# Kernel tuning notes

Hardware: AMD Instinct MI355X
Metric: run time of the kernel (lower is better)

## Reference

```python
import jax, jax.numpy as jnp
import numpy as np

B, S, DIM = 1, 4096, 4096
H, HL, D = 32, 8, 128          # query heads, kv heads (GQA), head_dim
BS = 8                          # sparse_block_size
SINK_TOK, WIN_TOK = 30, 30
HEAVY = 800                     # heavy_const -> Mb = HEAVY // BS top blocks
NEG = -1e30


def setup_inputs() -> dict:
    key = jax.random.key(0)
    k0, k1, k2, k3 = jax.random.split(key, 4)
    x = jax.random.normal(k0, (B, S, DIM), jnp.float32)
    freqs_cis = jax.random.uniform(k1, (S, D // 2, 2), jnp.float32)  # (cos,sin)-like pairs
    wqkv_w = jax.random.normal(k2, ((H + 2 * HL) * D, DIM), jnp.float32) * 0.02
    wo_w = jax.random.normal(k3, (DIM, DIM), jnp.float32) * 0.02
    input_pos = jnp.arange(S, dtype=jnp.int32)
    return {"x": x, "freqs_cis": freqs_cis, "wqkv_w": wqkv_w, "wo_w": wo_w, "input_pos": input_pos}


def _rope(x, fc):
    # x: [B,S,h,D], fc: [S,D/2,2]
    xr = x.reshape(*x.shape[:-1], -1, 2)            # [B,S,h,D/2,2]
    fc = fc[None, :, None]                           # [1,S,1,D/2,2]
    out = jnp.stack([xr[..., 0] * fc[..., 0] - xr[..., 1] * fc[..., 1],
                     xr[..., 1] * fc[..., 0] + xr[..., 0] * fc[..., 1]], axis=-1)
    return out.reshape(x.shape)


def reference(x, freqs_cis, wqkv_w, wo_w, input_pos):
    rep = H // HL
    Tb = (S + BS - 1) // BS
    scale = 1.0 / jnp.sqrt(jnp.float32(D))

    qkv = x @ wqkv_w.T                               # [B,S,(H+2HL)*D]
    q, k, v = jnp.split(qkv, [H * D, (H + HL) * D], axis=-1)
    q = q.reshape(B, S, H, D)
    k = k.reshape(B, S, HL, D)
    v = v.reshape(B, S, HL, D)
    q = _rope(q, freqs_cis)
    k = _rope(k, freqs_cis)

    # ---- block accumulators (KVCache.update_tokens), vectorized ----
    blk = input_pos // BS                            # [S]
    k_sum = jax.ops.segment_sum(jnp.swapaxes(k, 0, 1), blk, num_segments=Tb)  # [Tb,B,HL,D]
    cnt = jax.ops.segment_sum(jnp.ones((S,), jnp.float32), blk, num_segments=Tb)  # [Tb]
    k_rep = k_sum / jnp.maximum(cnt, 1.0)[:, None, None, None]                # block-mean keys
    k_rep_h = jnp.repeat(k_rep, rep, axis=2)        # [Tb,B,H,D] (GQA repeat)

    # ---- per-(B,H) block routing scores ----
    q_mean = q.mean(axis=1)                          # [B,H,D]
    scores = jnp.einsum('bhd,tbhd->bht', q_mean, k_rep_h) * scale  # [B,H,Tb]
    scores = jnp.where(cnt[None, None, :] > 0, scores, NEG)

    # ---- build_block_index: sink + window + topk ----
    sink_b = min((min(SINK_TOK, S) + BS - 1) // BS, Tb)
    window_b = min((min(WIN_TOK, S) + BS - 1) // BS, Tb)
    cur_block = (S - 1) // BS
    win_start = max(0, cur_block - window_b + 1)
    win_end = cur_block + 1
    sink_ids = jnp.arange(sink_b, dtype=jnp.int32)
    window_ids = jnp.arange(win_start, win_end, dtype=jnp.int32)
    Mb = max(0, min(HEAVY // BS, Tb))
    sc = scores.at[..., :sink_b].set(NEG).at[..., window_ids].set(NEG)
    top_ids = jax.lax.top_k(sc, Mb)[1].astype(jnp.int32)                      # [B,H,Mb]
    bidx = jnp.concatenate([
        jnp.broadcast_to(sink_ids, (B, H, sink_b)),
        jnp.broadcast_to(window_ids, (B, H, win_end - win_start)),
        top_ids], axis=-1)                           # [B,H,KLIST]

    # ---- gather selected block tokens ----
    tok = bidx[..., None] * BS + jnp.arange(BS, dtype=jnp.int32)              # [B,H,KLIST,BS]
    KL = bidx.shape[-1]
    tok = tok.reshape(B, H, KL * BS)                 # [B,H,Kt]
    valid = (tok >= 0) & (tok < S)
    tok_c = jnp.clip(tok, 0, S - 1)

    k_bhsd = jnp.swapaxes(jnp.repeat(k, rep, axis=2), 1, 2)  # [B,H,S,D]
    v_bhsd = jnp.swapaxes(jnp.repeat(v, rep, axis=2), 1, 2)
    Ksel = jnp.take_along_axis(k_bhsd, tok_c[..., None], axis=2)  # [B,H,Kt,D]
    Vsel = jnp.take_along_axis(v_bhsd, tok_c[..., None], axis=2)

    # ---- block-sparse attention with causal mask ----
    q_bhsd = jnp.swapaxes(q, 1, 2)                   # [B,H,S,D]
    att = jnp.einsum('bhsd,bhkd->bhsk', q_bhsd, Ksel) * scale
    mask = (tok_c[:, :, None, :] <= input_pos[None, None, :, None]) & valid[:, :, None, :]
    att = jnp.where(mask, att, NEG)
    p = jax.nn.softmax(att, axis=-1)
    out = jnp.einsum('bhsk,bhkd->bhsd', p, Vsel)     # [B,H,S,D]
    y = jnp.swapaxes(out, 1, 2).reshape(B, S, H * D) @ wo_w.T
    return y
```

## Files before the change

### kernel.cpp

```cpp
#include <hip/hip_runtime.h>
#include <hip/hip_bf16.h>

typedef unsigned short u16;
typedef unsigned int   u32;

using bf16x8 = __attribute__((ext_vector_type(8))) short;
using f32x4  = __attribute__((ext_vector_type(4))) float;

constexpr int S = 4096, DIM = 4096, H = 32, HL = 8, D = 128;
constexpr int NQKV = (H + 2 * HL) * D;
constexpr int QVW = (H + HL) * D;
constexpr int TB = S / 8;
constexpr int KL = 108;
constexpr float NEGF = -1e30f;
constexpr float SCALE = 0.08838834764831845f;

__device__ inline float bflo(u32 u) { return __builtin_bit_cast(float, u << 16); }
__device__ inline float bfhi(u32 u) { return __builtin_bit_cast(float, u & 0xFFFF0000u); }
__device__ inline u16 rne16(float f) {
  u32 b = __builtin_bit_cast(u32, f);
  return (u16)((b + 0x7FFFu + ((b >> 16) & 1u)) >> 16);
}
__device__ inline float bf2f(u16 h) { return __builtin_bit_cast(float, (u32)h << 16); }
__device__ inline u32 pk2(u16 a, u16 b) { return (u32)a | ((u32)b << 16); }

__device__ __forceinline__ void gload16(const u16* g, u16* l) {
  __builtin_amdgcn_global_load_lds(
      (__attribute__((address_space(1))) void*)g,
      (__attribute__((address_space(3))) void*)l, 16, 0, 0);
}

__device__ inline void xcd_swz(int nx, int& bx, int& by) {
  const int flat = blockIdx.y * nx + blockIdx.x;
  const int nwg = nx * gridDim.y;
  const int cpx = nwg >> 3;
  const int s = (flat & 7) * cpx + (flat >> 3);
  bx = s % nx;
  by = s / nx;
}

__global__ __launch_bounds__(256) void split_f32_kernel(
    const float* __restrict__ src, u16* __restrict__ hi, u16* __restrict__ lo) {
  const size_t i = ((size_t)blockIdx.x * 256 + threadIdx.x) * 8;
  float4 v0 = *(const float4*)(src + i);
  float4 v1 = *(const float4*)(src + i + 4);
  float f[8] = {v0.x, v0.y, v0.z, v0.w, v1.x, v1.y, v1.z, v1.w};
  u16 h[8], l[8];
#pragma unroll
  for (int j = 0; j < 8; ++j) {
    h[j] = rne16(f[j]);
    l[j] = rne16(f[j] - bf2f(h[j]));
  }
  uint4 ph, pl;
  ph.x = pk2(h[0], h[1]); ph.y = pk2(h[2], h[3]);
  ph.z = pk2(h[4], h[5]); ph.w = pk2(h[6], h[7]);
  pl.x = pk2(l[0], l[1]); pl.y = pk2(l[2], l[3]);
  pl.z = pk2(l[4], l[5]); pl.w = pk2(l[6], l[7]);
  *(uint4*)(hi + i) = ph;
  *(uint4*)(lo + i) = pl;
}

__global__ __launch_bounds__(256) void conv_wqkv_kernel(
    const float* __restrict__ src, u16* __restrict__ wqv,
    u16* __restrict__ wkh, u16* __restrict__ wkl) {
  const size_t i = ((size_t)blockIdx.x * 256 + threadIdx.x) * 8;
  float4 v0 = *(const float4*)(src + i);
  float4 v1 = *(const float4*)(src + i + 4);
  float f[8] = {v0.x, v0.y, v0.z, v0.w, v1.x, v1.y, v1.z, v1.w};
  u16 h[8];
#pragma unroll
  for (int j = 0; j < 8; ++j) h[j] = rne16(f[j]);
  uint4 ph;
  ph.x = pk2(h[0], h[1]); ph.y = pk2(h[2], h[3]);
  ph.z = pk2(h[4], h[5]); ph.w = pk2(h[6], h[7]);
  const int row = (int)(i >> 12);
  if (row < H * D) {
    *(uint4*)(wqv + i) = ph;
  } else if (row < (H + HL) * D) {
    const size_t off = i - (size_t)(H * D) * DIM;
    u16 l[8];
#pragma unroll
    for (int j = 0; j < 8; ++j) l[j] = rne16(f[j] - bf2f(h[j]));
    uint4 pl;
    pl.x = pk2(l[0], l[1]); pl.y = pk2(l[2], l[3]);
    pl.z = pk2(l[4], l[5]); pl.w = pk2(l[6], l[7]);
    *(uint4*)(wkh + off) = ph;
    *(uint4*)(wkl + off) = pl;
  } else {
    *(uint4*)(wqv + (i - (size_t)(HL * D) * DIM)) = ph;
  }
}

__global__ __launch_bounds__(256) void cast_bf16_kernel(
    const float* __restrict__ src, u16* __restrict__ dst) {
  const size_t i = ((size_t)blockIdx.x * 256 + threadIdx.x) * 8;
  float4 v0 = *(const float4*)(src + i);
  float4 v1 = *(const float4*)(src + i + 4);
  uint4 ph;
  ph.x = pk2(rne16(v0.x), rne16(v0.y));
  ph.y = pk2(rne16(v0.z), rne16(v0.w));
  ph.z = pk2(rne16(v1.x), rne16(v1.y));
  ph.w = pk2(rne16(v1.z), rne16(v1.w));
  *(uint4*)(dst + i) = ph;
}

template <bool OBF16>
__global__ __launch_bounds__(256) void gemm_bf16(
    const u16* __restrict__ A, const u16* __restrict__ B,
    void* __restrict__ Cp, int M, int N, int K, int lda, int ldb, int ldc) {
  __shared__ u16 As[2][128 * 32];
  __shared__ u16 Bs[2][128 * 32];
  const int tid = threadIdx.x;
  const int lane = tid & 63;
  const int w = tid >> 6;
  const int wm = w >> 1, wn = w & 1;
  int bx, by;
  xcd_swz(gridDim.x, bx, by);
  const int m0 = by * 128, n0 = bx * 128;
  const int l15 = lane & 15, g = lane >> 4;
  const int srow = tid >> 2;
  const int scol = (tid & 3) * 8;

  const u16* ga = A + (size_t)(m0 + srow) * lda + scol;
  const u16* gb = B + (size_t)(n0 + srow) * ldb + scol;
  const size_t a64 = (size_t)64 * lda;
  const size_t b64 = (size_t)64 * ldb;

  auto stage = [&](int buf, int k0) {
    u16* lA = As[buf] + w * 512;
    u16* lB = Bs[buf] + w * 512;
    gload16(ga + k0, lA);
    gload16(ga + k0 + a64, lA + 2048);
    gload16(gb + k0, lB);
    gload16(gb + k0 + b64, lB + 2048);
  };

  f32x4 acc[4][4];
#pragma unroll
  for (int i = 0; i < 4; ++i)
#pragma unroll
    for (int j = 0; j < 4; ++j) acc[i][j] = {0.f, 0.f, 0.f, 0.f};

  stage(0, 0);
  __syncthreads();
  const int niter = K / 32;
  for (int it = 0; it < niter; ++it) {
    const int cur = it & 1;
    if (it + 1 < niter) stage(cur ^ 1, (it + 1) * 32);
    bf16x8 af[4], bfr[4];
#pragma unroll
    for (int i = 0; i < 4; ++i)
      af[i] = *(const bf16x8*)(As[cur] + (wm * 64 + i * 16 + l15) * 32 + g * 8);
#pragma unroll
    for (int j = 0; j < 4; ++j)
      bfr[j] = *(const bf16x8*)(Bs[cur] + (wn * 64 + j * 16 + l15) * 32 + g * 8);
#pragma unroll
    for (int i = 0; i < 4; ++i)
#pragma unroll
      for (int j = 0; j < 4; ++j)
        acc[i][j] = __builtin_amdgcn_mfma_f32_16x16x32_bf16(af[i], bfr[j], acc[i][j], 0, 0, 0);
    __syncthreads();
  }
#pragma unroll
  for (int i = 0; i < 4; ++i)
#pragma unroll
    for (int j = 0; j < 4; ++j)
#pragma unroll
      for (int rg = 0; rg < 4; ++rg) {
        const int row = m0 + wm * 64 + i * 16 + g * 4 + rg;
        const int col = n0 + wn * 64 + j * 16 + l15;
        if constexpr (OBF16)
          ((u16*)Cp)[(size_t)row * ldc + col] = rne16(acc[i][j][rg]);
        else
          ((float*)Cp)[(size_t)row * ldc + col] = acc[i][j][rg];
      }
}

__global__ __launch_bounds__(256) void gemm_k3(
    const u16* __restrict__ Ahg, const u16* __restrict__ Alg,
    const u16* __restrict__ Bhg, const u16* __restrict__ Blg,
    float* __restrict__ C, int M, int N, int K) {
  __shared__ u16 Ah[2][128 * 32];
  __shared__ u16 Al[2][128 * 32];
  __shared__ u16 Bh[2][64 * 32];
  __shared__ u16 Bl[2][64 * 32];
  const int tid = threadIdx.x;
  const int lane = tid & 63;
  const int w = tid >> 6;
  const int wm = w >> 1, wn = w & 1;
  int bx, by;
  xcd_swz(gridDim.x, bx, by);
  const int m0 = by * 128, n0 = bx * 64;
  const int l15 = lane & 15, g = lane >> 4;
  const int srow = tid >> 2;
  const int scol = (tid & 3) * 8;

  const u16* gah = Ahg + (size_t)(m0 + srow) * K + scol;
  const u16* gal = Alg + (size_t)(m0 + srow) * K + scol;
  const u16* gbh = Bhg + (size_t)(n0 + srow) * K + scol;
  const u16* gbl = Blg + (size_t)(n0 + srow) * K + scol;
  const size_t a64 = (size_t)64 * K;

  auto stage = [&](int buf, int k0) {
    gload16(gah + k0, Ah[buf] + w * 512);
    gload16(gah + k0 + a64, Ah[buf] + w * 512 + 2048);
    gload16(gal + k0, Al[buf] + w * 512);
    gload16(gal + k0 + a64, Al[buf] + w * 512 + 2048);
    gload16(gbh + k0, Bh[buf] + w * 512);
    gload16(gbl + k0, Bl[buf] + w * 512);
  };

  f32x4 acc[4][2];
#pragma unroll
  for (int i = 0; i < 4; ++i)
#pragma unroll
    for (int j = 0; j < 2; ++j) acc[i][j] = {0.f, 0.f, 0.f, 0.f};

  stage(0, 0);
  __syncthreads();
  const int niter = K / 32;
  for (int it = 0; it < niter; ++it) {
    const int cur = it & 1;
    if (it + 1 < niter) stage(cur ^ 1, (it + 1) * 32);
    bf16x8 fah[4], fal[4], fbh[2], fbl[2];
#pragma unroll
    for (int i = 0; i < 4; ++i) {
      fah[i] = *(const bf16x8*)(Ah[cur] + (wm * 64 + i * 16 + l15) * 32 + g * 8);
      fal[i] = *(const bf16x8*)(Al[cur] + (wm * 64 + i * 16 + l15) * 32 + g * 8);
    }
#pragma unroll
    for (int j = 0; j < 2; ++j) {
      fbh[j] = *(const bf16x8*)(Bh[cur] + (wn * 32 + j * 16 + l15) * 32 + g * 8);
      fbl[j] = *(const bf16x8*)(Bl[cur] + (wn * 32 + j * 16 + l15) * 32 + g * 8);
    }
#pragma unroll
    for (int i = 0; i < 4; ++i)
#pragma unroll
      for (int j = 0; j < 2; ++j) {
        acc[i][j] = __builtin_amdgcn_mfma_f32_16x16x32_bf16(fal[i], fbh[j], acc[i][j], 0, 0, 0);
        acc[i][j] = __builtin_amdgcn_mfma_f32_16x16x32_bf16(fah[i], fbl[j], acc[i][j], 0, 0, 0);
        acc[i][j] = __builtin_amdgcn_mfma_f32_16x16x32_bf16(fah[i], fbh[j], acc[i][j], 0, 0, 0);
      }
    __syncthreads();
  }
#pragma unroll
  for (int i = 0; i < 4; ++i)
#pragma unroll
    for (int j = 0; j < 2; ++j)
#pragma unroll
      for (int rg = 0; rg < 4; ++rg) {
        const int row = m0 + wm * 64 + i * 16 + g * 4 + rg;
        const int col = n0 + wn * 32 + j * 16 + l15;
        C[(size_t)row * N + col] = acc[i][j][rg];
      }
}

__global__ __launch_bounds__(128) void xcd_kernel(
    const float* __restrict__ x, const float* __restrict__ freqs,
    float* __restrict__ XC, float* __restrict__ XD) {
  const int d = blockIdx.x * 128 + threadIdx.x;
  const int i0 = blockIdx.y * 32;
  const int s0 = blockIdx.z * 128;
  float accC[32], accD[32];
#pragma unroll
  for (int ii = 0; ii < 32; ++ii) { accC[ii] = 0.f; accD[ii] = 0.f; }
  for (int s = s0; s < s0 + 128; ++s) {
    const float xv = x[(size_t)s * DIM + d];
    const float* fr = freqs + (size_t)s * 128 + i0 * 2;
#pragma unroll
    for (int ii = 0; ii < 32; ++ii) {
      accC[ii] += fr[2 * ii] * xv;
      accD[ii] += fr[2 * ii + 1] * xv;
    }
  }
#pragma unroll
  for (int ii = 0; ii < 32; ++ii) {
    atomicAdd(&XC[(size_t)(i0 + ii) * DIM + d], accC[ii]);
    atomicAdd(&XD[(size_t)(i0 + ii) * DIM + d], accD[ii]);
  }
}

__global__ __launch_bounds__(256) void mrow_kernel(
    const float* __restrict__ wq, const float* __restrict__ XC,
    const float* __restrict__ XD, float* __restrict__ M1, float* __restrict__ M2) {
  const int r = blockIdx.x * 4 + (threadIdx.x >> 6);
  const int lane = threadIdx.x & 63;
  const int i = (r & 127) >> 1;
  const float* wr = wq + (size_t)r * DIM;
  const float* xc = XC + (size_t)i * DIM;
  const float* xd = XD + (size_t)i * DIM;
  float s1 = 0.f, s2 = 0.f;
  for (int k = lane; k < DIM; k += 64) {
    float wv = wr[k];
    s1 += wv * xc[k];
    s2 += wv * xd[k];
  }
#pragma unroll
  for (int off = 1; off < 64; off <<= 1) {
    s1 += __shfl_xor(s1, off, 64);
    s2 += __shfl_xor(s2, off, 64);
  }
  if (lane == 0) { M1[r] = s1; M2[r] = s2; }
}

__global__ __launch_bounds__(256) void rope_q_kernel(
    const u16* __restrict__ qvb, const float* __restrict__ freqs,
    u16* __restrict__ qb) {
  const int h = blockIdx.y;
  const int s0 = blockIdx.x * 64;
  const int tid = threadIdx.x;
  const int d = tid & 127, half = tid >> 7;
  for (int pp = half; pp < 64; pp += 2) {
    const int s = s0 + pp;
    u32 pr = *(const u32*)(qvb + (size_t)s * QVW + h * D + (d & ~1));
    float a = bflo(pr), b = bfhi(pr);
    float2 fc = *(const float2*)(freqs + (size_t)s * 128 + (d & ~1));
    float o = (d & 1) ? (b * fc.x + a * fc.y) : (a * fc.x - b * fc.y);
    qb[((size_t)h * S + s) * D + d] = rne16(o);
  }
}

__global__ __launch_bounds__(128) void rope_kv_kernel(
    const float* __restrict__ kf, const u16* __restrict__ qvb,
    const float* __restrict__ freqs,
    u16* __restrict__ kb, u16* __restrict__ vbt, float* __restrict__ krep) {
  const int hl = blockIdx.y;
  const int t = blockIdx.x;
  const int d = threadIdx.x;
  float sum = 0.f;
  u16 vv[8];
#pragma unroll
  for (int pp = 0; pp < 8; ++pp) {
    const int s = t * 8 + pp;
    float2 kp = *(const float2*)(kf + (size_t)s * 1024 + hl * D + (d & ~1));
    float2 fc = *(const float2*)(freqs + (size_t)s * 128 + (d & ~1));
    float o = (d & 1) ? (kp.y * fc.x + kp.x * fc.y) : (kp.x * fc.x - kp.y * fc.y);
    kb[((size_t)hl * S + s) * D + d] = rne16(o);
    sum += o;
    vv[pp] = qvb[(size_t)s * QVW + H * D + hl * D + d];
  }
  krep[((size_t)t * HL + hl) * D + d] = sum * 0.125f;
  uint4 pk;
  pk.x = pk2(vv[0], vv[1]);
  pk.y = pk2(vv[2], vv[3]);
  pk.z = pk2(vv[4], vv[5]);
  pk.w = pk2(vv[6], vv[7]);
  *(uint4*)(vbt + ((size_t)hl * D + d) * S + t * 8) = pk;
}

__global__ __launch_bounds__(512) void topk_kernel(
    const float* __restrict__ M1, const float* __restrict__ M2,
    const float* __restrict__ krep, int* __restrict__ bidx) {
  const int h = blockIdx.x;
  const int t = threadIdx.x;
  __shared__ float qm[128];
  if (t < 128) {
    int r = h * 128 + t;
    float v = (t & 1) ? (M1[r] + M2[r - 1]) : (M1[r] - M2[r + 1]);
    qm[t] = v * (1.f / 4096.f);
  }
  __syncthreads();
  const float* kr = krep + ((size_t)t * HL + (h >> 2)) * 128;
  float s = 0.f;
#pragma unroll 8
  for (int d = 0; d < 128; ++d) s += qm[d] * kr[d];
  s *= SCALE;
  if (t < 4 || t >= 508) s = NEGF;
  if (t < 4) {
    bidx[h * KL + t] = t;
    bidx[h * KL + 4 + t] = 508 + t;
  }
  __shared__ float wv[8];
  __shared__ int wi[8];
  __shared__ int bestsh;
  for (int iter = 0; iter < 100; ++iter) {
    float v = s;
    int idx = t;
#pragma unroll
    for (int off = 1; off < 64; off <<= 1) {
      float ov = __shfl_xor(v, off, 64);
      int oi = __shfl_xor(idx, off, 64);
      if (ov > v || (ov == v && oi < idx)) { v = ov; idx = oi; }
    }
    if ((t & 63) == 0) { wv[t >> 6] = v; wi[t >> 6] = idx; }
    __syncthreads();
    if (t == 0) {
      float bv = wv[0];
      int bi = wi[0];
#pragma unroll
      for (int u = 1; u < 8; ++u)
        if (wv[u] > bv || (wv[u] == bv && wi[u] < bi)) { bv = wv[u]; bi = wi[u]; }
      bestsh = bi;
      bidx[h * KL + 8 + iter] = bi;
    }
    __syncthreads();
    if (t == bestsh) s = NEGF;
  }
}

__global__ __launch_bounds__(256) void attn_mfma(
    const u16* __restrict__ qb, const u16* __restrict__ kb,
    const u16* __restrict__ vbt, const int* __restrict__ bidx,
    u16* __restrict__ attno) {
  __shared__ u16 Ks[32][136];
  __shared__ u16 Vt[128][40];
  __shared__ u16 Ps[4][16][40];
  const int h = blockIdx.y, hl = h >> 2;
  const int q0 = blockIdx.x * 64;
  const int tid = threadIdx.x;
  const int w = tid >> 6, lane = tid & 63;
  const int l15 = lane & 15, g = lane >> 4;

  bf16x8 qf[4];
  {
    const u16* qp = qb + ((size_t)h * S + q0 + w * 16 + l15) * D + g * 8;
#pragma unroll
    for (int c = 0; c < 4; ++c) qf[c] = *(const bf16x8*)(qp + c * 32);
  }
  f32x4 o[8];
#pragma unroll
  for (int c = 0; c < 8; ++c) o[c] = {0.f, 0.f, 0.f, 0.f};
  float mrow[4], lrow[4];
#pragma unroll
  for (int r = 0; r < 4; ++r) { mrow[r] = NEGF; lrow[r] = 0.f; }

  for (int step = 0; step < KL / 4; ++step) {
    const int b0 = bidx[h * KL + step * 4 + 0];
    const int b1 = bidx[h * KL + step * 4 + 1];
    const int b2 = bidx[h * KL + step * 4 + 2];
    const int b3 = bidx[h * KL + step * 4 + 3];
    {
      const int tok = tid >> 3, seg = tid & 7;
      const int blk = (tok < 8) ? b0 : (tok < 16) ? b1 : (tok < 24) ? b2 : b3;
      const u16* src = kb + ((size_t)hl * S + blk * 8 + (tok & 7)) * D + seg * 16;
      *(uint4*)&Ks[tok][seg * 16] = *(const uint4*)src;
      *(uint4*)&Ks[tok][seg * 16 + 8] = *(const uint4*)(src + 8);
    }
    {
      const int d = tid >> 1, hf = tid & 1;
      const int ba = hf ? b2 : b0, bb = hf ? b3 : b1;
      const u16* src = vbt + ((size_t)hl * D + d) * S;
      *(uint4*)&Vt[d][hf * 16] = *(const uint4*)(src + ba * 8);
      *(uint4*)&Vt[d][hf * 16 + 8] = *(const uint4*)(src + bb * 8);
    }
    __syncthreads();
    f32x4 sA = {0.f, 0.f, 0.f, 0.f}, sB = {0.f, 0.f, 0.f, 0.f};
#pragma unroll
    for (int c = 0; c < 4; ++c) {
      bf16x8 k0 = *(const bf16x8*)&Ks[l15][c * 32 + g * 8];
      bf16x8 k1 = *(const bf16x8*)&Ks[16 + l15][c * 32 + g * 8];
      sA = __builtin_amdgcn_mfma_f32_16x16x32_bf16(qf[c], k0, sA, 0, 0, 0);
      sB = __builtin_amdgcn_mfma_f32_16x16x32_bf16(qf[c], k1, sB, 0, 0, 0);
    }
    const int tgA = ((l15 < 8) ? b0 : b1) * 8 + (l15 & 7);
    const int tgB = ((l15 < 8) ? b2 : b3) * 8 + (l15 & 7);
    float pA[4], pB[4], alpha[4];
#pragma unroll
    for (int r = 0; r < 4; ++r) {
      const int sq = q0 + w * 16 + g * 4 + r;
      pA[r] = (tgA <= sq) ? sA[r] * SCALE : NEGF;
      pB[r] = (tgB <= sq) ? sB[r] * SCALE : NEGF;
      float mx = fmaxf(pA[r], pB[r]);
      mx = fmaxf(mx, __shfl_xor(mx, 1, 64));
      mx = fmaxf(mx, __shfl_xor(mx, 2, 64));
      mx = fmaxf(mx, __shfl_xor(mx, 4, 64));
      mx = fmaxf(mx, __shfl_xor(mx, 8, 64));
      const float mnew = fmaxf(mrow[r], mx);
      alpha[r] = __expf(mrow[r] - mnew);
      mrow[r] = mnew;
      pA[r] = __expf(pA[r] - mnew);
      pB[r] = __expf(pB[r] - mnew);
      float rs = pA[r] + pB[r];
      rs += __shfl_xor(rs, 1, 64);
      rs += __shfl_xor(rs, 2, 64);
      rs += __shfl_xor(rs, 4, 64);
      rs += __shfl_xor(rs, 8, 64);
      lrow[r] = lrow[r] * alpha[r] + rs;
    }
#pragma unroll
    for (int c = 0; c < 8; ++c) {
      o[c][0] *= alpha[0]; o[c][1] *= alpha[1];
      o[c][2] *= alpha[2]; o[c][3] *= alpha[3];
    }
#pragma unroll
    for (int r = 0; r < 4; ++r) {
      Ps[w][g * 4 + r][l15] = rne16(pA[r]);
      Ps[w][g * 4 + r][16 + l15] = rne16(pB[r]);
    }
    bf16x8 pf = *(const bf16x8*)&Ps[w][l15][g * 8];
#pragma unroll
    for (int c = 0; c < 8; ++c) {
      bf16x8 vf = *(const bf16x8*)&Vt[c * 16 + l15][g * 8];
      o[c] = __builtin_amdgcn_mfma_f32_16x16x32_bf16(pf, vf, o[c], 0, 0, 0);
    }
    __syncthreads();
  }
  float inv[4];
#pragma unroll
  for (int r = 0; r < 4; ++r) inv[r] = 1.f / lrow[r];
#pragma unroll
  for (int c = 0; c < 8; ++c)
#pragma unroll
    for (int r = 0; r < 4; ++r)
      attno[(size_t)(q0 + w * 16 + g * 4 + r) * DIM + h * D + c * 16 + l15] =
          rne16(o[c][r] * inv[r]);
}

extern "C" void kernel_launch(void* const* d_in, const int* in_sizes, int n_in,
                              void* d_out, int out_size, void* d_ws, size_t ws_size,
                              hipStream_t stream) {
  const float* x     = (const float*)d_in[0];
  const float* freqs = (const float*)d_in[1];
  const float* wqkv  = (const float*)d_in[2];
  const float* wo    = (const float*)d_in[3];
  float* out = (float*)d_out;

  char* p = (char*)d_ws;
  auto alloc = [&](size_t bytes) {
    char* r = p;
    p += (bytes + 255) & ~(size_t)255;
    return r;
  };
  u16*   xh   = (u16*)alloc((size_t)S * DIM * 2);
  u16*   xl   = (u16*)alloc((size_t)S * DIM * 2);
  u16*   wqv  = (u16*)alloc((size_t)QVW * DIM * 2);
  u16*   wkh  = (u16*)alloc((size_t)HL * D * DIM * 2);
  u16*   wkl  = (u16*)alloc((size_t)HL * D * DIM * 2);
  u16*   wob  = (u16*)alloc((size_t)DIM * DIM * 2);
  u16*   qvb  = (u16*)alloc((size_t)S * QVW * 2);
  float* kf32 = (float*)alloc((size_t)S * HL * D * 4);
  u16*   qb   = (u16*)alloc((size_t)H * S * D * 2);
  u16*   kb   = (u16*)alloc((size_t)HL * S * D * 2);
  u16*   vbt  = (u16*)alloc((size_t)HL * D * S * 2);
  float* krep = (float*)alloc((size_t)TB * HL * D * 4);
  float* XC   = (float*)alloc((size_t)64 * DIM * 4);
  float* XD   = (float*)alloc((size_t)64 * DIM * 4);
  float* M1   = (float*)alloc((size_t)H * D * 4);
  float* M2   = (float*)alloc((size_t)H * D * 4);
  int*   bidx = (int*)alloc((size_t)H * KL * 4);
  u16*   attno = (u16*)alloc((size_t)S * DIM * 2);

  hipMemsetAsync(XC, 0, (size_t)64 * DIM * 4, stream);
  hipMemsetAsync(XD, 0, (size_t)64 * DIM * 4, stream);

  split_f32_kernel<<<(S * DIM) / 2048, 256, 0, stream>>>(x, xh, xl);
  conv_wqkv_kernel<<<(NQKV * DIM) / 2048, 256, 0, stream>>>(wqkv, wqv, wkh, wkl);
  cast_bf16_kernel<<<(DIM * DIM) / 2048, 256, 0, stream>>>(wo, wob);

  gemm_bf16<true><<<dim3(QVW / 128, S / 128), 256, 0, stream>>>(
      xh, wqv, qvb, S, QVW, DIM, DIM, DIM, QVW);

  gemm_k3<<<dim3((HL * D) / 64, S / 128), 256, 0, stream>>>(
      xh, xl, wkh, wkl, kf32, S, HL * D, DIM);

  xcd_kernel<<<dim3(32, 2, 32), 128, 0, stream>>>(x, freqs, XC, XD);
  mrow_kernel<<<1024, 256, 0, stream>>>(wqkv, XC, XD, M1, M2);
  rope_q_kernel<<<dim3(S / 64, H), 256, 0, stream>>>(qvb, freqs, qb);
  rope_kv_kernel<<<dim3(TB, HL), 128, 0, stream>>>(kf32, qvb, freqs, kb, vbt, krep);
  topk_kernel<<<H, 512, 0, stream>>>(M1, M2, krep, bidx);
  attn_mfma<<<dim3(S / 64, H), 256, 0, stream>>>(qb, kb, vbt, bidx, attno);
  gemm_bf16<false><<<dim3(DIM / 128, S / 128), 256, 0, stream>>>(
      attno, wob, out, S, DIM, DIM, DIM, DIM, DIM);
}
```

Before: 1.308 ms.

## Add 256x256-tile bf16 GEMM with 8 waves for Q and output projections

Introduces a new GEMM kernel with 256x256 output tiles, 512 threads, swizzled LDS staging via direct global-to-LDS loads, interleaved fragment loads and MFMA phases, and raised wave priority during MFMA. It is used for the Q part of the QKV projection and for the output projection, and the V part is split off into a separate launch of the old 128-tile kernel. Larger tiles raise arithmetic intensity and cut global traffic per FLOP. The cost is fewer blocks (256 for a 4096x4096 output), which may underfill the GPU's CUs, plus higher register pressure from the 128-float accumulator per thread.

Result: faster. 1.267 ms (-3.1%).

```diff
diff --git a/kernel.cpp b/kernel.cpp
--- a/kernel.cpp
+++ b/kernel.cpp
@@ -102,6 +102,129 @@
   ph.z = pk2(rne16(v1.x), rne16(v1.y));
   ph.w = pk2(rne16(v1.z), rne16(v1.w));
   *(uint4*)(dst + i) = ph;
+}
+
+template <bool OBF16>
+__global__ __launch_bounds__(512, 2) void gemm256(
+    const u16* __restrict__ A, const u16* __restrict__ B,
+    void* __restrict__ Cp, int M, int N, int K, int lda, int ldb, int ldc) {
+  __shared__ u16 lds[4 * 16384];
+  const int tid = threadIdx.x;
+  const int w = tid >> 6, lane = tid & 63;
+  const int wm = w >> 2, wn = w & 3;
+  const int l15 = lane & 15, g = lane >> 4;
+  int bx, by;
+  xcd_swz(gridDim.x, bx, by);
+  const int m0 = by * 256, n0 = bx * 256;
+
+  const u16* ga[4];
+  const u16* gb[4];
+#pragma unroll
+  for (int r = 0; r < 4; ++r) {
+    const int c = r * 512 + tid;
+    const int row = c >> 3, j = c & 7;
+    const int jsw = j ^ (row & 7);
+    ga[r] = A + (size_t)(m0 + row) * lda + jsw * 8;
+    gb[r] = B + (size_t)(n0 + row) * ldb + jsw * 8;
+  }
+
+  auto stageA = [&](int buf, int kt) {
+    u16* base = lds + buf * 32768 + w * 512;
+#pragma unroll
+    for (int r = 0; r < 4; ++r) gload16(ga[r] + kt * 64, base + r * 4096);
+  };
+  auto stageB = [&](int buf, int kt) {
+    u16* base = lds + buf * 32768 + 16384 + w * 512;
+#pragma unroll
+    for (int r = 0; r < 4; ++r) gload16(gb[r] + kt * 64, base + r * 4096);
+  };
+
+  bf16x8 afr[4][2], bfr[2][2];
+  auto loadA = [&](int buf, int q) {
+    const u16* Ab = lds + buf * 32768;
+#pragma unroll
+    for (int fr = 0; fr < 4; ++fr) {
+      const int row = wm * 128 + q * 64 + fr * 16 + l15;
+#pragma unroll
+      for (int kh = 0; kh < 2; ++kh)
+        afr[fr][kh] = *(const bf16x8*)(Ab + row * 64 + ((((kh << 2) | g)) ^ (l15 & 7)) * 8);
+    }
+  };
+  auto loadB = [&](int buf, int r2) {
+    const u16* Bb = lds + buf * 32768 + 16384;
+#pragma unroll
+    for (int fc = 0; fc < 2; ++fc) {
+      const int row = wn * 64 + r2 * 32 + fc * 16 + l15;
+#pragma unroll
+      for (int kh = 0; kh < 2; ++kh)
+        bfr[fc][kh] = *(const bf16x8*)(Bb + row * 64 + ((((kh << 2) | g)) ^ (l15 & 7)) * 8);
+    }
+  };
+
+  f32x4 acc[8][4];
+#pragma unroll
+  for (int i = 0; i < 8; ++i)
+#pragma unroll
+    for (int j = 0; j < 4; ++j) acc[i][j] = {0.f, 0.f, 0.f, 0.f};
+
+  auto mma = [&](int q, int r2) {
+    __builtin_amdgcn_s_setprio(1);
+#pragma unroll
+    for (int fr = 0; fr < 4; ++fr)
+#pragma unroll
+      for (int fc = 0; fc < 2; ++fc)
+#pragma unroll
+        for (int kh = 0; kh < 2; ++kh)
+          acc[q * 4 + fr][r2 * 2 + fc] = __builtin_amdgcn_mfma_f32_16x16x32_bf16(
+              afr[fr][kh], bfr[fc][kh], acc[q * 4 + fr][r2 * 2 + fc], 0, 0, 0);
+    __builtin_amdgcn_s_setprio(0);
+  };
+
+  stageA(0, 0);
+  stageB(0, 0);
+  const int NT = K / 64;
+  for (int t = 0; t < NT; ++t) {
+    const int cur = t & 1, nxt = cur ^ 1;
+    if (t + 1 < NT) {
+      stageA(nxt, t + 1);
+      asm volatile("s_waitcnt vmcnt(4)" ::: "memory");
+    } else {
+      asm volatile("s_waitcnt vmcnt(0)" ::: "memory");
+    }
+    __builtin_amdgcn_sched_barrier(0);
+    __builtin_amdgcn_s_barrier();
+    loadA(cur, 0);
+    loadB(cur, 0);
+    mma(0, 0);
+    __builtin_amdgcn_s_barrier();
+    loadA(cur, 1);
+    if (t + 1 < NT) stageB(nxt, t + 1);
+    __builtin_amdgcn_s_barrier();
+    mma(1, 0);
+    __builtin_amdgcn_s_barrier();
+    loadA(cur, 0);
+    loadB(cur, 1);
+    __builtin_amdgcn_s_barrier();
+    mma(0, 1);
+    __builtin_amdgcn_s_barrier();
+    loadA(cur, 1);
+    __builtin_amdgcn_s_barrier();
+    mma(1, 1);
+    __builtin_amdgcn_s_barrier();
+  }
+#pragma unroll
+  for (int mf = 0; mf < 8; ++mf)
+#pragma unroll
+    for (int nf = 0; nf < 4; ++nf)
+#pragma unroll
+      for (int rg = 0; rg < 4; ++rg) {
+        const int row = m0 + wm * 128 + mf * 16 + g * 4 + rg;
+        const int col = n0 + wn * 64 + nf * 16 + l15;
+        if constexpr (OBF16)
+          ((u16*)Cp)[(size_t)row * ldc + col] = rne16(acc[mf][nf][rg]);
+        else
+          ((float*)Cp)[(size_t)row * ldc + col] = acc[mf][nf][rg];
+      }
 }
 
 template <bool OBF16>
@@ -547,8 +670,10 @@
   conv_wqkv_kernel<<<(NQKV * DIM) / 2048, 256, 0, stream>>>(wqkv, wqv, wkh, wkl);
   cast_bf16_kernel<<<(DIM * DIM) / 2048, 256, 0, stream>>>(wo, wob);
 
-  gemm_bf16<true><<<dim3(QVW / 128, S / 128), 256, 0, stream>>>(
-      xh, wqv, qvb, S, QVW, DIM, DIM, DIM, QVW);
+  gemm256<true><<<dim3((H * D) / 256, S / 256), 512, 0, stream>>>(
+      xh, wqv, qvb, S, H * D, DIM, DIM, DIM, QVW);
+  gemm_bf16<true><<<dim3((HL * D) / 128, S / 128), 256, 0, stream>>>(
+      xh, wqv + (size_t)(H * D) * DIM, qvb + H * D, S, HL * D, DIM, DIM, DIM, QVW);
 
   gemm_k3<<<dim3((HL * D) / 64, S / 128), 256, 0, stream>>>(
       xh, xl, wkh, wkl, kf32, S, HL * D, DIM);
@@ -559,6 +684,6 @@
   rope_kv_kernel<<<dim3(TB, HL), 128, 0, stream>>>(kf32, qvb, freqs, kb, vbt, krep);
   topk_kernel<<<H, 512, 0, stream>>>(M1, M2, krep, bidx);
   attn_mfma<<<dim3(S / 64, H), 256, 0, stream>>>(qb, kb, vbt, bidx, attno);
-  gemm_bf16<false><<<dim3(DIM / 128, S / 128), 256, 0, stream>>>(
+  gemm256<false><<<dim3(DIM / 256, S / 256), 512, 0, stream>>>(
       attno, wob, out, S, DIM, DIM, DIM, DIM, DIM);
 }
```
